# Optimization experiments

Measured on AMD Instinct MI355X. Metric: run time of the kernel, lower is better.

## Reference

```python
import jax, jax.numpy as jnp
import numpy as np

N_HEADS = 16
HEAD_SIZE = 64
EMBED = 1024
BLOCK = 2048
B, T = 2, 2048


def setup_inputs() -> dict:
    key = jax.random.key(0)
    ks = jax.random.split(key, 6)
    scale = 0.02
    inputs = jax.random.normal(ks[0], (B, T, EMBED), dtype=jnp.float32)
    # per-head projection weights, stacked: [H, E, D]
    Wk = jax.random.normal(ks[1], (N_HEADS, EMBED, HEAD_SIZE), dtype=jnp.float32) * scale
    Wq = jax.random.normal(ks[2], (N_HEADS, EMBED, HEAD_SIZE), dtype=jnp.float32) * scale
    Wv = jax.random.normal(ks[3], (N_HEADS, EMBED, HEAD_SIZE), dtype=jnp.float32) * scale
    Wo = jax.random.normal(ks[4], (EMBED, EMBED), dtype=jnp.float32) * scale
    bo = jax.random.normal(ks[5], (EMBED,), dtype=jnp.float32) * scale
    return {"inputs": inputs, "Wk": Wk, "Wq": Wq, "Wv": Wv, "Wo": Wo, "bo": bo}


def reference(inputs, Wk, Wq, Wv, Wo, bo):
    # per-head projections: [B,H,T,D]
    k = jnp.einsum("bte,hed->bhtd", inputs, Wk)
    q = jnp.einsum("bte,hed->bhtd", inputs, Wq)
    v = jnp.einsum("bte,hed->bhtd", inputs, Wv)
    # NOTE: original computes wei = K @ Q^T (faithful reproduction)
    wei = jnp.einsum("bhtd,bhsd->bhts", k, q) * (HEAD_SIZE ** -0.5)
    causal = jnp.tril(jnp.ones((T, T), dtype=bool))  # tril==0 masked
    wei = jnp.where(causal, wei, -jnp.inf)
    wei = jax.nn.softmax(wei, axis=-1)
    out = jnp.einsum("bhts,bhsd->bhtd", wei, v)
    # concat heads along feature dim: [B,T,H*D]
    z = out.transpose(0, 2, 1, 3).reshape(B, T, N_HEADS * HEAD_SIZE)
    z = z @ Wo.T + bo  # match torch Linear(x) = x @ W^T + b
    return z
```

## Files before the change

### kernel.cpp

```cpp
#include <hip/hip_runtime.h>
#include <cstdint>
#include <cstddef>

typedef __bf16 bf8_t __attribute__((ext_vector_type(8)));
typedef float  f4_t  __attribute__((ext_vector_type(4)));
typedef unsigned u32x2_t __attribute__((ext_vector_type(2)));

static __device__ __forceinline__ f4_t mfma16(bf8_t a, bf8_t b, f4_t c) {
    return __builtin_amdgcn_mfma_f32_16x16x32_bf16(a, b, c, 0, 0, 0);
}

#if defined(__has_builtin) && __has_builtin(__builtin_amdgcn_exp2f)
#define EXP2F(x) __builtin_amdgcn_exp2f(x)
#else
#define EXP2F(x) exp2f(x)
#endif

static __device__ __forceinline__ void plane32swap(unsigned& a, unsigned& b) {
#if defined(__has_builtin) && __has_builtin(__builtin_amdgcn_permlane32_swap)
    u32x2_t r = __builtin_amdgcn_permlane32_swap(a, b, false, false);
    a = r[0]; b = r[1];
#else
    unsigned ax = __shfl_xor(a, 32);
    unsigned bx = __shfl_xor(b, 32);
    bool hi = ((threadIdx.x & 63) >= 32);
    unsigned na = hi ? bx : a;
    unsigned nb = hi ? b : ax;
    a = na; b = nb;
#endif
}

static __device__ __forceinline__ unsigned pack2(float a, float b) {
    __bf16 lo = (__bf16)a, hi = (__bf16)b;
    unsigned short ulo = __builtin_bit_cast(unsigned short, lo);
    unsigned short uhi = __builtin_bit_cast(unsigned short, hi);
    return (unsigned)ulo | ((unsigned)uhi << 16);
}

static __device__ __forceinline__ void async_ld16(const __bf16* g, __bf16* l) {
    __builtin_amdgcn_global_load_lds(
        (const __attribute__((address_space(1))) void*)(uintptr_t)g,
        (__attribute__((address_space(3))) void*)(uintptr_t)l, 16, 0, 0);
}


__global__ void __launch_bounds__(256) prep_all(const float* __restrict__ X,
                                                const float* __restrict__ Wo,
                                                const float* __restrict__ Wq,
                                                const float* __restrict__ Wk,
                                                const float* __restrict__ Wv,
                                                __bf16* __restrict__ Xbf,
                                                __bf16* __restrict__ Wobf,
                                                __bf16* __restrict__ Wqt,
                                                __bf16* __restrict__ Wkt,
                                                __bf16* __restrict__ Wvt,
                                                int* __restrict__ ctrs) {
    __shared__ float tile[64][65];
    int bx = (int)blockIdx.x;
    if (bx == 0 && threadIdx.x < 128) ctrs[threadIdx.x] = 0;
    if (bx < 2560) {
        const float* src; __bf16* dst; size_t base;
        if (bx < 2048) { src = X;  dst = Xbf;  base = (size_t)bx * 2048; }
        else           { src = Wo; dst = Wobf; base = (size_t)(bx - 2048) * 2048; }
        size_t i = base + (size_t)threadIdx.x * 8;
        float4 a = *(const float4*)(src + i);
        float4 b = *(const float4*)(src + i + 4);
        bf8_t o;
        o[0] = (__bf16)a.x; o[1] = (__bf16)a.y; o[2] = (__bf16)a.z; o[3] = (__bf16)a.w;
        o[4] = (__bf16)b.x; o[5] = (__bf16)b.y; o[6] = (__bf16)b.z; o[7] = (__bf16)b.w;
        *(bf8_t*)(dst + i) = o;
        return;
    }
    int wt = bx - 2560;
    int which = wt >> 8, inner = wt & 255;
    const float* W; __bf16* Wt;
    if (which == 0)      { W = Wq; Wt = Wqt; }
    else if (which == 1) { W = Wk; Wt = Wkt; }
    else                 { W = Wv; Wt = Wvt; }
    int h = inner >> 4, eb = inner & 15;
    int tx = threadIdx.x;
    int e = tx >> 2, dg = (tx & 3) * 16;
    const float* src = W + ((size_t)h * 1024 + eb * 64 + e) * 64 + dg;
#pragma unroll
    for (int i = 0; i < 4; ++i) {
        float4 v = *(const float4*)(src + i * 4);
        tile[dg + i * 4 + 0][e] = v.x;
        tile[dg + i * 4 + 1][e] = v.y;
        tile[dg + i * 4 + 2][e] = v.z;
        tile[dg + i * 4 + 3][e] = v.w;
    }
    __syncthreads();
    int d = tx >> 2, eg = (tx & 3) * 16;
    __bf16* dst = Wt + (size_t)(h * 64 + d) * 1024 + eb * 64 + eg;
    bf8_t o0, o1;
#pragma unroll
    for (int i = 0; i < 8; ++i) o0[i] = (__bf16)tile[d][eg + i];
#pragma unroll
    for (int i = 0; i < 8; ++i) o1[i] = (__bf16)tile[d][eg + 8 + i];
    *(bf8_t*)dst       = o0;
    *(bf8_t*)(dst + 8) = o1;
}

static __device__ __forceinline__ void gemm_tile128(const __bf16* __restrict__ A,
                                                    const __bf16* __restrict__ Bt,
                                                    __bf16* As, __bf16* Bs,
                                                    int m0, int n0, f4_t acc[4][4]) {
    const int tid  = threadIdx.x;
    const int lane = tid & 63;
    const int wv   = tid >> 6;
    const int lrow = lane >> 3;
    const int lsc  = lane & 7;
    const int quad = lane >> 4;
    const int l15  = lane & 15;
    const int wm = (wv & 1) * 64;
    const int wn = (wv >> 1) * 64;
    f4_t zero = {0.f, 0.f, 0.f, 0.f};
#pragma unroll
    for (int mi = 0; mi < 4; ++mi)
#pragma unroll
        for (int ni = 0; ni < 4; ++ni) acc[mi][ni] = zero;

    for (int kb = 0; kb < 16; ++kb) {
#pragma unroll
        for (int j = 0; j < 4; ++j) {
            int row = wv * 32 + j * 8 + lrow;
            int lc  = lsc ^ (row & 7);
            async_ld16(A + (size_t)(m0 + row) * 1024 + kb * 64 + lc * 8,
                       As + (wv * 32 + j * 8) * 64);
            async_ld16(Bt + (size_t)(n0 + row) * 1024 + kb * 64 + lc * 8,
                       Bs + (wv * 32 + j * 8) * 64);
        }
        __syncthreads();
#pragma unroll
        for (int ks = 0; ks < 2; ++ks) {
            bf8_t af[4], bfr[4];
#pragma unroll
            for (int mi = 0; mi < 4; ++mi) {
                int row = wm + mi * 16 + l15;
                int ch  = (ks * 4 + quad) ^ (row & 7);
                af[mi] = *(const bf8_t*)(As + row * 64 + ch * 8);
            }
#pragma unroll
            for (int ni = 0; ni < 4; ++ni) {
                int row = wn + ni * 16 + l15;
                int ch  = (ks * 4 + quad) ^ (row & 7);
                bfr[ni] = *(const bf8_t*)(Bs + row * 64 + ch * 8);
            }
#pragma unroll
            for (int mi = 0; mi < 4; ++mi)
#pragma unroll
                for (int ni = 0; ni < 4; ++ni)
                    acc[mi][ni] = mfma16(af[mi], bfr[ni], acc[mi][ni]);
        }
        __syncthreads();
    }
}

__global__ void __launch_bounds__(256, 3) gemm_proj(const __bf16* __restrict__ Xbf,
                                                    const __bf16* __restrict__ Wqt,
                                                    const __bf16* __restrict__ Wkt,
                                                    const __bf16* __restrict__ Wvt,
                                                    __bf16* __restrict__ Qb,
                                                    __bf16* __restrict__ Kb,
                                                    __bf16* __restrict__ Vt) {
    __shared__ __bf16 smem[17408];
    __bf16* As = smem;
    __bf16* Bs = smem + 8192;
    int which = blockIdx.y;
    const __bf16* Bt = which == 0 ? Wqt : (which == 1 ? Wkt : Wvt);
    int bx = (int)blockIdx.x;
    int xcd = bx & 7, qq = bx >> 3;
    int m0 = (xcd * 4 + (qq & 3)) * 128;
    int n0 = (qq >> 2) * 128;
    f4_t acc[4][4];
    gemm_tile128(Xbf, Bt, As, Bs, m0, n0, acc);
    const int lane = threadIdx.x & 63, wv = threadIdx.x >> 6;
    const int quad = lane >> 4, l15 = lane & 15;
    const int wm = (wv & 1) * 64, wn = (wv >> 1) * 64;
    const int STR = 136;
    if (which < 2) {
        __bf16* C = which ? Kb : Qb;
        const float scl = which ? 0.18033688f : 1.0f;
#pragma unroll
        for (int mi = 0; mi < 4; ++mi)
#pragma unroll
            for (int ni = 0; ni < 4; ++ni)
#pragma unroll
                for (int r = 0; r < 4; ++r) {
                    int ml = wm + mi * 16 + quad * 4 + r;
                    int nl = wn + ni * 16 + l15;
                    smem[ml * STR + nl] = (__bf16)(acc[mi][ni][r] * scl);
                }
        __syncthreads();
        int row = (int)threadIdx.x >> 1;
        int seg = (int)threadIdx.x & 1;
        int m = m0 + row;
        int b = m >> 11, t = m & 2047;
        int h = (n0 >> 6) + seg;
        __bf16* dst = C + ((size_t)(b * 16 + h) * 2048 + t) * 64;
        const __bf16* srcl = smem + row * STR + seg * 64;
#pragma unroll
        for (int k = 0; k < 8; ++k)
            *(bf8_t*)(dst + k * 8) = *(const bf8_t*)(srcl + k * 8);
    } else {
#pragma unroll
        for (int mi = 0; mi < 4; ++mi)
#pragma unroll
            for (int ni = 0; ni < 4; ++ni)
#pragma unroll
                for (int r = 0; r < 4; ++r) {
                    int ml = wm + mi * 16 + quad * 4 + r;
                    int nl = wn + ni * 16 + l15;
                    smem[nl * STR + ml] = (__bf16)acc[mi][ni][r];
                }
        __syncthreads();
        int b = m0 >> 11, tg0 = m0 & 2047;
        int nl = (int)threadIdx.x >> 1;
        int tc = ((int)threadIdx.x & 1) * 64;
        int n = n0 + nl, h = n >> 6, d = n & 63;
        __bf16* dst = Vt + ((size_t)(b * 16 + h) * 64 + d) * 2048 + tg0 + tc;
        const __bf16* srcl = smem + nl * STR + tc;
#pragma unroll
        for (int k = 0; k < 8; ++k)
            *(bf8_t*)(dst + k * 8) = *(const bf8_t*)(srcl + k * 8);
    }
}

static __device__ __forceinline__ void gemm_tile(const __bf16* __restrict__ A,
                                                 const __bf16* __restrict__ Bt,
                                                 __bf16* As, __bf16* Bs,
                                                 int m0, int n0, f4_t acc[4][2]) {
    const int tid  = threadIdx.x;
    const int lane = tid & 63;
    const int wv   = tid >> 6;
    const int lrow = lane >> 3;
    const int lsc  = lane & 7;
    const int quad = lane >> 4;
    const int l15  = lane & 15;
    const int wm = (wv & 1) * 64;
    const int wn = (wv >> 1) * 32;
    f4_t zero = {0.f, 0.f, 0.f, 0.f};
#pragma unroll
    for (int mi = 0; mi < 4; ++mi)
#pragma unroll
        for (int ni = 0; ni < 2; ++ni) acc[mi][ni] = zero;

    for (int kb = 0; kb < 16; ++kb) {
#pragma unroll
        for (int j = 0; j < 4; ++j) {
            int row = wv * 32 + j * 8 + lrow;
            int lc  = lsc ^ (row & 7);
            async_ld16(A + (size_t)(m0 + row) * 1024 + kb * 64 + lc * 8,
                       As + (wv * 32 + j * 8) * 64);
        }
#pragma unroll
        for (int j = 0; j < 2; ++j) {
            int row = wv * 16 + j * 8 + lrow;
            int lc  = lsc ^ (row & 7);
            async_ld16(Bt + (size_t)(n0 + row) * 1024 + kb * 64 + lc * 8,
                       Bs + (wv * 16 + j * 8) * 64);
        }
        __syncthreads();
#pragma unroll
        for (int ks = 0; ks < 2; ++ks) {
            bf8_t af[4], bfr[2];
#pragma unroll
            for (int mi = 0; mi < 4; ++mi) {
                int row = wm + mi * 16 + l15;
                int ch  = (ks * 4 + quad) ^ (row & 7);
                af[mi] = *(const bf8_t*)(As + row * 64 + ch * 8);
            }
#pragma unroll
            for (int ni = 0; ni < 2; ++ni) {
                int row = wn + ni * 16 + l15;
                int ch  = (ks * 4 + quad) ^ (row & 7);
                bfr[ni] = *(const bf8_t*)(Bs + row * 64 + ch * 8);
            }
#pragma unroll
            for (int mi = 0; mi < 4; ++mi)
#pragma unroll
                for (int ni = 0; ni < 2; ++ni)
                    acc[mi][ni] = mfma16(af[mi], bfr[ni], acc[mi][ni]);
        }
        __syncthreads();
    }
}

__global__ void __launch_bounds__(256) gemm_out(const __bf16* __restrict__ Ob,
                                                const __bf16* __restrict__ Wobf,
                                                const float* __restrict__ bo,
                                                float* __restrict__ out) {
    __shared__ __bf16 smem[128 * 64 + 64 * 64];
    __bf16* As = smem;
    __bf16* Bs = smem + 128 * 64;
    int bx = (int)blockIdx.x;
    int xcd = bx & 7, qq = bx >> 3;
    int m0 = (xcd * 4 + (qq & 3)) * 128;
    int n0 = (qq >> 2) * 64;
    f4_t acc[4][2];
    gemm_tile(Ob, Wobf, As, Bs, m0, n0, acc);
    const int lane = threadIdx.x & 63, wv = threadIdx.x >> 6;
    const int quad = lane >> 4, l15 = lane & 15;
    const int wm = (wv & 1) * 64, wn = (wv >> 1) * 32;
#pragma unroll
    for (int mi = 0; mi < 4; ++mi)
#pragma unroll
        for (int ni = 0; ni < 2; ++ni)
#pragma unroll
            for (int r = 0; r < 4; ++r) {
                int m = m0 + wm + mi * 16 + quad * 4 + r;
                int n = n0 + wn + ni * 16 + l15;
                out[(size_t)m * 1024 + n] = acc[mi][ni][r] + bo[n];
            }
}

__device__ const unsigned char ITEMS[48] = {
    124, 125, 121, 62,
    120, 116, 117, 113, 58,
    112, 108, 109, 105, 54,
    104, 100, 101, 97, 50,
    96, 92, 93, 89, 46,
    88, 84, 85, 81, 42,
    80, 76, 77, 73, 38,
    72, 68, 69, 65, 34,
    64, 30,
    26, 22, 18, 14, 10, 6, 2
};
__global__ void __launch_bounds__(256, 4) attn(const __bf16* __restrict__ Kb,
                                               const __bf16* __restrict__ Qb,
                                               const __bf16* __restrict__ Vt,
                                               __bf16* __restrict__ Ob,
                                               __bf16* __restrict__ Opart,
                                               float* __restrict__ Lpart,
                                               int* __restrict__ ctrs) {
    __shared__ __bf16 Qs[2][64 * 64];
    __shared__ __bf16 Vs[2][64 * 64];
    __shared__ int item_lds;
    const int tid = threadIdx.x, lane = tid & 63, wv = tid >> 6;
    const int quad = lane >> 4, l15 = lane & 15;
    const int lrow8 = lane >> 3, lchunk = lane & 7;
    const bool qodd = (quad & 1) != 0;
    int xcc;
    asm volatile("s_getreg_b32 %0, hwreg(HW_REG_XCC_ID)" : "=s"(xcc));
    xcc &= 7;
    int* ctr = ctrs + xcc * 16;
    f4_t zero = {0.f, 0.f, 0.f, 0.f};

    for (;;) {
        if (tid == 0) item_lds = atomicAdd(ctr, 1);
        __syncthreads();
        const int q = item_lds;
        if (q >= 192) break;
        const int code = ITEMS[q >> 2];
        const int tt = code >> 2, c = code & 3;
        const int bh = xcc * 4 + (q & 3);
        const int b = bh >> 4, h = bh & 15;
        const int t0 = tt * 64;
        const int tw = t0 + wv * 16;
        const int sMid = (tt + 1) >> 1;
        const int sLo = (c == 1) ? sMid : 0;
        const int sHi = (c == 0) ? sMid : tt + 1;
        const __bf16* Kp = Kb + (size_t)bh * 2048 * 64;
        const __bf16* Qp = Qb + (size_t)bh * 2048 * 64;
        const __bf16* Vp = Vt + (size_t)bh * 64 * 2048;

        bf8_t kfrag[2];
#pragma unroll
        for (int ks = 0; ks < 2; ++ks)
            kfrag[ks] = *(const bf8_t*)(Kp + (size_t)(tw + l15) * 64 + ks * 32 + quad * 8);

        f4_t oacc[4];
#pragma unroll
        for (int ni = 0; ni < 4; ++ni) oacc[ni] = zero;
        float lsum = 0.f;

        auto stage = [&](int buf, int s0) {
#pragma unroll
            for (int j = 0; j < 2; ++j) {
                int row = wv * 8 + j * 32 + lrow8;
                int cg  = lchunk ^ (row & 7);
                async_ld16(Qp + (size_t)(s0 + row) * 64 + cg * 8,
                           &Qs[buf][(wv * 8 + j * 32) * 64]);
                async_ld16(Vp + (size_t)row * 2048 + s0 + cg * 8,
                           &Vs[buf][(wv * 8 + j * 32) * 64]);
            }
        };

        stage(sLo & 1, sLo * 64);
        for (int sb = sLo; sb < sHi; ++sb) {
            const int cur = sb & 1;
            const int s0 = sb * 64;
            const bool masked = (sb == tt);
            __syncthreads();
            if (sb + 1 < sHi) stage(1 ^ cur, s0 + 64);
            const __bf16* Qc = &Qs[cur][0];
            const __bf16* Vc = &Vs[cur][0];
            f4_t sacc[4] = {zero, zero, zero, zero};
            __builtin_amdgcn_s_setprio(1);
#pragma unroll
            for (int ks = 0; ks < 2; ++ks) {
                bf8_t qf[4];
#pragma unroll
                for (int st = 0; st < 4; ++st) {
                    int row = st * 16 + l15;
                    int ch  = (ks * 4 + quad) ^ (row & 7);
                    qf[st] = *(const bf8_t*)(Qc + row * 64 + ch * 8);
                }
#pragma unroll
                for (int st = 0; st < 4; ++st)
                    sacc[st] = mfma16(qf[st], kfrag[ks], sacc[st]);
            }
            __builtin_amdgcn_s_setprio(0);
            const int lim = tw + l15 - s0;
#pragma unroll
            for (int st = 0; st < 4; ++st)
#pragma unroll
                for (int r = 0; r < 4; ++r) {
                    float e = EXP2F(sacc[st][r]);
                    if (masked && (st * 16 + quad * 4 + r > lim)) e = 0.0f;
                    lsum += e;
                    sacc[st][r] = e;
                }
            unsigned pk[4][2];
#pragma unroll
            for (int st = 0; st < 4; ++st)
#pragma unroll
                for (int rp = 0; rp < 2; ++rp)
                    pk[st][rp] = pack2(sacc[st][2 * rp], sacc[st][2 * rp + 1]);
            bf8_t pf[2];
#pragma unroll
            for (int ks = 0; ks < 2; ++ks) {
                unsigned w0, w1, w2, w3;
                {
                    unsigned A = pk[2 * ks][0], B = pk[2 * ks + 1][0];
                    plane32swap(A, B);
                    unsigned As_ = __shfl_xor(A, 16);
                    unsigned Bs_ = __shfl_xor(B, 16);
                    w0 = qodd ? Bs_ : A;
                    w2 = qodd ? B : As_;
                }
                {
                    unsigned A = pk[2 * ks][1], B = pk[2 * ks + 1][1];
                    plane32swap(A, B);
                    unsigned As_ = __shfl_xor(A, 16);
                    unsigned Bs_ = __shfl_xor(B, 16);
                    w1 = qodd ? Bs_ : A;
                    w3 = qodd ? B : As_;
                }
                union { unsigned u[4]; bf8_t v; } cv;
                cv.u[0] = w0; cv.u[1] = w1; cv.u[2] = w2; cv.u[3] = w3;
                pf[ks] = cv.v;
            }
            __builtin_amdgcn_s_setprio(1);
#pragma unroll
            for (int ks = 0; ks < 2; ++ks) {
                bf8_t vf[4];
#pragma unroll
                for (int ni = 0; ni < 4; ++ni) {
                    int row = ni * 16 + l15;
                    int ch  = (ks * 4 + quad) ^ (row & 7);
                    vf[ni] = *(const bf8_t*)(Vc + row * 64 + ch * 8);
                }
#pragma unroll
                for (int ni = 0; ni < 4; ++ni)
                    oacc[ni] = mfma16(pf[ks], vf[ni], oacc[ni]);
            }
            __builtin_amdgcn_s_setprio(0);
        }

        float l = lsum;
        l += __shfl_xor(l, 16);
        l += __shfl_xor(l, 32);
        if (c != 2) {
            if (quad == 0)
                Lpart[c * 32768 + bh * 1024 + (tw - 1024) + l15] = l;
            size_t pb = (size_t)(c * 32 + bh) * 1024 + (tw - 1024);
#pragma unroll
            for (int r = 0; r < 4; ++r)
#pragma unroll
                for (int ni = 0; ni < 4; ++ni)
                    Opart[(pb + quad * 4 + r) * 64 + ni * 16 + l15] =
                        (__bf16)oacc[ni][r];
        } else {
            float inv = 1.0f / l;
#pragma unroll
            for (int r = 0; r < 4; ++r) {
                float invr = __shfl(inv, quad * 4 + r);
                int t = tw + quad * 4 + r;
#pragma unroll
                for (int ni = 0; ni < 4; ++ni)
                    Ob[((size_t)(b * 2048 + t) * 16 + h) * 64 + ni * 16 + l15] =
                        (__bf16)(oacc[ni][r] * invr);
            }
        }
    }
}

__global__ void __launch_bounds__(256) attn_merge(const __bf16* __restrict__ Opart,
                                                  const float* __restrict__ Lpart,
                                                  __bf16* __restrict__ Ob) {
    int gid = (int)blockIdx.x * 256 + (int)threadIdx.x;
    int bh = gid >> 13;
    int rem = gid & 8191;
    int tl = rem >> 3;
    int dg = (rem & 7) * 8;
    float l0 = Lpart[bh * 1024 + tl];
    float l1 = Lpart[32768 + bh * 1024 + tl];
    float inv = 1.0f / (l0 + l1);
    bf8_t a = *(const bf8_t*)(Opart + ((size_t)bh * 1024 + tl) * 64 + dg);
    bf8_t c = *(const bf8_t*)(Opart + ((size_t)(32 + bh) * 1024 + tl) * 64 + dg);
    bf8_t o;
#pragma unroll
    for (int i = 0; i < 8; ++i)
        o[i] = (__bf16)(((float)a[i] + (float)c[i]) * inv);
    int b = bh >> 4, h = bh & 15, t = 1024 + tl;
    *(bf8_t*)(Ob + ((size_t)(b * 2048 + t) * 16 + h) * 64 + dg) = o;
}

extern "C" void kernel_launch(void* const* d_in, const int* in_sizes, int n_in,
                              void* d_out, int out_size, void* d_ws, size_t ws_size,
                              hipStream_t stream) {
    const float* X  = (const float*)d_in[0];
    const float* Wk = (const float*)d_in[1];
    const float* Wq = (const float*)d_in[2];
    const float* Wv = (const float*)d_in[3];
    const float* Wo = (const float*)d_in[4];
    const float* bo = (const float*)d_in[5];
    float* out = (float*)d_out;

    __bf16* ws   = (__bf16*)d_ws;
    __bf16* Xbf  = ws;
    __bf16* Wqt  = ws + 4194304;
    __bf16* Wkt  = ws + 5242880;
    __bf16* Wvt  = ws + 6291456;
    __bf16* Wobf = ws + 7340032;
    __bf16* Qb   = ws + 8388608;
    __bf16* Kb   = ws + 12582912;
    __bf16* Vt   = ws + 16777216;
    __bf16* Ob   = ws + 20971520;
    float*  Lpart = (float*)(ws + 1048576);
    __bf16* Opart = ws + 2097152;
    int* ctrs = (int*)out;

    prep_all<<<3328, 256, 0, stream>>>(X, Wo, Wq, Wk, Wv, Xbf, Wobf, Wqt, Wkt, Wvt, ctrs);
    gemm_proj<<<dim3(256, 3), 256, 0, stream>>>(Xbf, Wqt, Wkt, Wvt, Qb, Kb, Vt);
    attn<<<768, 256, 0, stream>>>(Kb, Qb, Vt, Ob, Opart, Lpart, ctrs);
    attn_merge<<<1024, 256, 0, stream>>>(Opart, Lpart, Ob);
    gemm_out<<<512, 256, 0, stream>>>(Ob, Wobf, bo, out);
}
```

Measured before the change: 173.3 us.

## Fuse split-KV attention merge into output projection GEMM A-tile load

Removes the separate attn_merge kernel. For rows in the second half of each sequence, the output GEMM now reads both partial attention outputs and the per-row softmax denominators, combines and normalises them, and writes the result straight into the shared-memory A tile. This saves one launch and a write plus re-read of the merged Ob region. In exchange, those blocks use synchronous loads with VALU work instead of async copies, which may hurt latency hiding in the GEMM main loop. The counter-clear in prep_all also now zeroes 1024 entries instead of 128.

After: 185.6 us. 7.1% more time.

```diff
diff --git a/kernel.cpp b/kernel.cpp
--- a/kernel.cpp
+++ b/kernel.cpp
@@ -57,7 +57,10 @@
                                                 int* __restrict__ ctrs) {
     __shared__ float tile[64][65];
     int bx = (int)blockIdx.x;
-    if (bx == 0 && threadIdx.x < 128) ctrs[threadIdx.x] = 0;
+    if (bx == 0) {
+#pragma unroll
+        for (int k = 0; k < 4; ++k) ctrs[(int)threadIdx.x * 4 + k] = 0;
+    }
     if (bx < 2560) {
         const float* src; __bf16* dst; size_t base;
         if (bx < 2048) { src = X;  dst = Xbf;  base = (size_t)bx * 2048; }
@@ -226,10 +229,20 @@
     }
 }
 
-static __device__ __forceinline__ void gemm_tile(const __bf16* __restrict__ A,
-                                                 const __bf16* __restrict__ Bt,
-                                                 __bf16* As, __bf16* Bs,
-                                                 int m0, int n0, f4_t acc[4][2]) {
+__global__ void __launch_bounds__(256) gemm_out(const __bf16* __restrict__ Ob,
+                                                const __bf16* __restrict__ Opart,
+                                                const float* __restrict__ Lpart,
+                                                const __bf16* __restrict__ Wobf,
+                                                const float* __restrict__ bo,
+                                                float* __restrict__ out) {
+    __shared__ __bf16 smem[128 * 64 + 64 * 64];
+    __shared__ float invsh[2048];
+    __bf16* As = smem;
+    __bf16* Bs = smem + 128 * 64;
+    int bx = (int)blockIdx.x;
+    int xcd = bx & 7, qq = bx >> 3;
+    int m0 = (xcd * 4 + (qq & 3)) * 128;
+    int n0 = (qq >> 2) * 64;
     const int tid  = threadIdx.x;
     const int lane = tid & 63;
     const int wv   = tid >> 6;
@@ -239,25 +252,54 @@
     const int l15  = lane & 15;
     const int wm = (wv & 1) * 64;
     const int wn = (wv >> 1) * 32;
+    const bool heavy = (m0 & 1024) != 0;
+    const int tbase = (m0 & 2047) - 1024;
+    const int bbase = (m0 >> 11) * 16;
+    if (heavy) {
+        for (int i = tid; i < 2048; i += 256) {
+            int hh = i >> 7, rr = i & 127;
+            int idx = (bbase + hh) * 1024 + tbase + rr;
+            invsh[i] = 1.0f / (Lpart[idx] + Lpart[32768 + idx]);
+        }
+        __syncthreads();
+    }
     f4_t zero = {0.f, 0.f, 0.f, 0.f};
+    f4_t acc[4][2];
 #pragma unroll
     for (int mi = 0; mi < 4; ++mi)
 #pragma unroll
         for (int ni = 0; ni < 2; ++ni) acc[mi][ni] = zero;
 
     for (int kb = 0; kb < 16; ++kb) {
-#pragma unroll
-        for (int j = 0; j < 4; ++j) {
-            int row = wv * 32 + j * 8 + lrow;
-            int lc  = lsc ^ (row & 7);
-            async_ld16(A + (size_t)(m0 + row) * 1024 + kb * 64 + lc * 8,
-                       As + (wv * 32 + j * 8) * 64);
+        if (heavy) {
+#pragma unroll
+            for (int j = 0; j < 4; ++j) {
+                int row = wv * 32 + j * 8 + lrow;
+                int lc  = lsc ^ (row & 7);
+                size_t po = ((size_t)(bbase + kb) * 1024 + tbase + row) * 64 + lc * 8;
+                bf8_t a0 = *(const bf8_t*)(Opart + po);
+                bf8_t a1 = *(const bf8_t*)(Opart + 2097152 + po);
+                float inv = invsh[kb * 128 + row];
+                bf8_t o;
+#pragma unroll
+                for (int i2 = 0; i2 < 8; ++i2)
+                    o[i2] = (__bf16)(((float)a0[i2] + (float)a1[i2]) * inv);
+                *(bf8_t*)(As + (wv * 32 + j * 8) * 64 + lane * 8) = o;
+            }
+        } else {
+#pragma unroll
+            for (int j = 0; j < 4; ++j) {
+                int row = wv * 32 + j * 8 + lrow;
+                int lc  = lsc ^ (row & 7);
+                async_ld16(Ob + (size_t)(m0 + row) * 1024 + kb * 64 + lc * 8,
+                           As + (wv * 32 + j * 8) * 64);
+            }
         }
 #pragma unroll
         for (int j = 0; j < 2; ++j) {
             int row = wv * 16 + j * 8 + lrow;
             int lc  = lsc ^ (row & 7);
-            async_ld16(Bt + (size_t)(n0 + row) * 1024 + kb * 64 + lc * 8,
+            async_ld16(Wobf + (size_t)(n0 + row) * 1024 + kb * 64 + lc * 8,
                        Bs + (wv * 16 + j * 8) * 64);
         }
         __syncthreads();
@@ -284,24 +326,6 @@
         }
         __syncthreads();
     }
-}
-
-__global__ void __launch_bounds__(256) gemm_out(const __bf16* __restrict__ Ob,
-                                                const __bf16* __restrict__ Wobf,
-                                                const float* __restrict__ bo,
-                                                float* __restrict__ out) {
-    __shared__ __bf16 smem[128 * 64 + 64 * 64];
-    __bf16* As = smem;
-    __bf16* Bs = smem + 128 * 64;
-    int bx = (int)blockIdx.x;
-    int xcd = bx & 7, qq = bx >> 3;
-    int m0 = (xcd * 4 + (qq & 3)) * 128;
-    int n0 = (qq >> 2) * 64;
-    f4_t acc[4][2];
-    gemm_tile(Ob, Wobf, As, Bs, m0, n0, acc);
-    const int lane = threadIdx.x & 63, wv = threadIdx.x >> 6;
-    const int quad = lane >> 4, l15 = lane & 15;
-    const int wm = (wv & 1) * 64, wn = (wv >> 1) * 32;
 #pragma unroll
     for (int mi = 0; mi < 4; ++mi)
 #pragma unroll
@@ -496,27 +520,6 @@
     }
 }
 
-__global__ void __launch_bounds__(256) attn_merge(const __bf16* __restrict__ Opart,
-                                                  const float* __restrict__ Lpart,
-                                                  __bf16* __restrict__ Ob) {
-    int gid = (int)blockIdx.x * 256 + (int)threadIdx.x;
-    int bh = gid >> 13;
-    int rem = gid & 8191;
-    int tl = rem >> 3;
-    int dg = (rem & 7) * 8;
-    float l0 = Lpart[bh * 1024 + tl];
-    float l1 = Lpart[32768 + bh * 1024 + tl];
-    float inv = 1.0f / (l0 + l1);
-    bf8_t a = *(const bf8_t*)(Opart + ((size_t)bh * 1024 + tl) * 64 + dg);
-    bf8_t c = *(const bf8_t*)(Opart + ((size_t)(32 + bh) * 1024 + tl) * 64 + dg);
-    bf8_t o;
-#pragma unroll
-    for (int i = 0; i < 8; ++i)
-        o[i] = (__bf16)(((float)a[i] + (float)c[i]) * inv);
-    int b = bh >> 4, h = bh & 15, t = 1024 + tl;
-    *(bf8_t*)(Ob + ((size_t)(b * 2048 + t) * 16 + h) * 64 + dg) = o;
-}
-
 extern "C" void kernel_launch(void* const* d_in, const int* in_sizes, int n_in,
                               void* d_out, int out_size, void* d_ws, size_t ws_size,
                               hipStream_t stream) {
@@ -545,6 +548,5 @@
     prep_all<<<3328, 256, 0, stream>>>(X, Wo, Wq, Wk, Wv, Xbf, Wobf, Wqt, Wkt, Wvt, ctrs);
     gemm_proj<<<dim3(256, 3), 256, 0, stream>>>(Xbf, Wqt, Wkt, Wvt, Qb, Kb, Vt);
     attn<<<768, 256, 0, stream>>>(Kb, Qb, Vt, Ob, Opart, Lpart, ctrs);
-    attn_merge<<<1024, 256, 0, stream>>>(Opart, Lpart, Ob);
-    gemm_out<<<512, 256, 0, stream>>>(Ob, Wobf, bo, out);
-}
+    gemm_out<<<512, 256, 0, stream>>>(Ob, Opart, Lpart, Wobf, bo, out);
+}
```
